# Kernel tuning notes

Hardware: AMD Instinct MI355X
Metric: run time of the kernel (lower is better)

## Reference

```python
import jax, jax.numpy as jnp
import numpy as np

B = 1024
IN_SHAPE = ((8, 8, 8), (8, 8))
IN_RANKS = ((32, 32, 32), (32, 32))
OUT_SHAPE = (16, 16, 16)
OUT_RANK = (32, 32, 32)


def _xavier(key, shape):
    # xavier_normal over axes [0,1] (in) and [2] (out), matching the torch helper
    fan_in = shape[0] * shape[1]
    fan_out = shape[2]
    std = float(np.sqrt(2.0 / (fan_in + fan_out)))
    return jax.random.normal(key, shape, dtype=jnp.float32) * std


def setup_inputs() -> dict:
    key = jax.random.key(0)
    ks = jax.random.split(key, 12)
    x_dims = tuple(d for g in IN_SHAPE for d in g)
    inp = {"x": jax.random.normal(ks[0], (B,) + x_dims, dtype=jnp.float32)}
    # input TT factors, flattened over groups in order (group, mode)
    fac_shapes = []
    for shapes, ranks in zip(IN_SHAPE, IN_RANKS):
        for i in range(len(shapes)):
            r_prev = 1 if i == 0 else ranks[i - 1]
            fac_shapes.append((r_prev, shapes[i], ranks[i]))
    for idx, fs in enumerate(fac_shapes):
        inp[f"f{idx}"] = _xavier(ks[1 + idx], fs)
    # core: (last rank of each group..., output_rank[-1])
    core_shape = tuple(r[-1] for r in IN_RANKS) + (OUT_RANK[-1],)
    fan_in = int(np.prod(core_shape[:-1]))
    std = float(np.sqrt(2.0 / (fan_in + core_shape[-1])))
    inp["core"] = jax.random.normal(ks[6], core_shape, dtype=jnp.float32) * std
    # output TT factors
    for i in range(len(OUT_SHAPE)):
        r_prev = 1 if i == 0 else OUT_RANK[i - 1]
        inp[f"g{i}"] = _xavier(ks[7 + i], (r_prev, OUT_SHAPE[i], OUT_RANK[i]))
    # bias: uniform(-1/sqrt(fan_in), +) with fan_in = total input features
    total_in = int(np.prod([np.prod(s) for s in IN_SHAPE]))
    bound = 1.0 / float(np.sqrt(total_in))
    inp["bias"] = jax.random.uniform(ks[10], OUT_SHAPE, dtype=jnp.float32,
                                     minval=-bound, maxval=bound)
    return inp


def reference(x, f0, f1, f2, f3, f4, core, g0, g1, g2, bias):
    groups = ((f0, f1, f2), (f3, f4))
    Bsz = x.shape[0]
    # T: [B, remaining_modes_flat, accumulated_group_ranks_flat]
    T = x.reshape(Bsz, -1)[:, :, None]
    for facs in groups:
        first = facs[0][0]                       # squeeze dummy rank-1: [n, r]
        n = first.shape[0]
        T = T.reshape(Bsz, n, -1, T.shape[-1])   # [B, n, M', Racc]
        T = jnp.einsum("bnmq,nr->bmqr", T, first)  # [B, M', Racc, r]
        for f in facs[1:]:
            n = f.shape[1]
            T = T.reshape(Bsz, n, -1, T.shape[-2], T.shape[-1])
            T = jnp.einsum("bnmqp,pnr->bmqr", T, f)
        # fold this group's final rank into the accumulated rank axis
        T = T.reshape(Bsz, T.shape[1], -1)
    # all input modes consumed -> T is [B, 1, r1_last*r2_last]
    z = T.reshape(Bsz, -1) @ core.reshape(-1, core.shape[-1])  # [B, Rout]
    # output TT chain -> W[o0, o1, o2, R_last]
    W = g0[0]
    for g in (g1, g2):
        W = jnp.einsum("...p,poq->...oq", W, g)
    R = W.shape[-1]
    out = z @ W.reshape(-1, R).T                 # [B, prod(OUT_SHAPE)]
    out = out.reshape((Bsz,) + OUT_SHAPE)
    return out + bias
```

## Files before the change

### kernel.cpp

```cpp
#include <hip/hip_runtime.h>

#define WS_M2 0
#define WS_N2 16384
#define WS_WT 18432
#define WS_Z  149504

__global__ __launch_bounds__(256) void precompute_kernel(
    const float* __restrict__ f0, const float* __restrict__ f1,
    const float* __restrict__ f2, const float* __restrict__ f3,
    const float* __restrict__ f4, const float* __restrict__ g0,
    const float* __restrict__ g1, const float* __restrict__ g2,
    float* __restrict__ ws)
{
    __shared__ float sA[8192];
    const int t = threadIdx.x;
    const int blk = blockIdx.x;
    if (blk < 8) {
        for (int i = t; i < 2048; i += 256) {
            int a01 = i >> 5, r2 = i & 31;
            int a0 = a01 >> 3, a1 = a01 & 7;
            float s = 0.f;
            #pragma unroll
            for (int r1 = 0; r1 < 32; ++r1)
                s += f0[a0*32 + r1] * f1[r1*256 + a1*32 + r2];
            sA[i] = s;
        }
        __syncthreads();
        for (int i = t; i < 2048; i += 256) {
            int a012 = blk*64 + (i >> 5), r3 = i & 31;
            int a01 = a012 >> 3, a2 = a012 & 7;
            float s = 0.f;
            #pragma unroll
            for (int r2 = 0; r2 < 32; ++r2)
                s += sA[a01*32 + r2] * f2[r2*256 + a2*32 + r3];
            ws[WS_M2 + a012*32 + r3] = s;
        }
    } else if (blk == 8) {
        for (int i = t; i < 2048; i += 256) {
            int a34 = i >> 5, s2 = i & 31;
            int a3 = a34 >> 3, a4 = a34 & 7;
            float s = 0.f;
            #pragma unroll
            for (int s1 = 0; s1 < 32; ++s1)
                s += f3[a3*32 + s1] * f4[s1*256 + a4*32 + s2];
            ws[WS_N2 + i] = s;
        }
    } else {
        const int j = blk - 9;
        for (int i = t; i < 8192; i += 256) {
            int o01 = i >> 5, q = i & 31;
            int o0 = o01 >> 4, o1 = o01 & 15;
            float s = 0.f;
            #pragma unroll
            for (int p = 0; p < 32; ++p)
                s += g0[o0*32 + p] * g1[p*512 + o1*32 + q];
            sA[i] = s;
        }
        __syncthreads();
        for (int i = t; i < 4096; i += 256) {
            int o = j*128 + (i >> 5);
            int r = i & 31;
            int o01 = o >> 4, o2 = o & 15;
            float s = 0.f;
            #pragma unroll
            for (int q = 0; q < 32; ++q)
                s += sA[o01*32 + q] * g2[q*512 + o2*32 + r];
            ws[WS_WT + r*4096 + o] = s;
        }
    }
}

__global__ __launch_bounds__(256, 4) void main_kernel(
    const float* __restrict__ x, const float* __restrict__ core,
    const float* __restrict__ ws, float* __restrict__ zout)
{
    __shared__ float buf[8320];
    __shared__ float spart[512];
    const int t = threadIdx.x;
    const int b = blockIdx.x;
    const int w    = __builtin_amdgcn_readfirstlane(t >> 6);
    const int lane = t & 63;

    const float* __restrict__ xw = x + (size_t)b * 32768 + w * 8192 + lane;
    const float* __restrict__ m2 = ws + WS_M2 + w * 4096;

    float acc[32];
    #pragma unroll
    for (int r = 0; r < 32; ++r) acc[r] = 0.f;

    for (int k0 = 0; k0 < 128; k0 += 8) {
        float xv[8];
        #pragma unroll
        for (int i = 0; i < 8; ++i) xv[i] = xw[(k0 + i) * 64];
        #pragma unroll
        for (int i = 0; i < 8; ++i) {
            const float* __restrict__ mr = m2 + (k0 + i) * 32;
            #pragma unroll
            for (int r = 0; r < 32; ++r) acc[r] += xv[i] * mr[r];
        }
    }

    #pragma unroll
    for (int r = 0; r < 32; ++r) buf[w*2080 + r*65 + lane] = acc[r];
    __syncthreads();

    {
        const int rr = t >> 3;
        const int mb = (t & 7) * 8;
        float s[8];
        #pragma unroll
        for (int i = 0; i < 8; ++i) {
            s[i] = buf[rr*65 + mb + i] + buf[2080 + rr*65 + mb + i]
                 + buf[4160 + rr*65 + mb + i] + buf[6240 + rr*65 + mb + i];
        }
        #pragma unroll
        for (int i = 0; i < 8; ++i) buf[rr*65 + mb + i] = s[i];
    }
    __syncthreads();

    {
        const float4* n24 = (const float4*)(ws + WS_N2);
        float4* d = (float4*)(buf + 4160);
        d[t] = n24[t];
        d[256 + t] = n24[256 + t];
    }
    __syncthreads();

    {
        const int r3  = t >> 3;
        const int s2b = (t & 7) * 4;
        float a0=0.f, a1=0.f, a2=0.f, a3=0.f;
        #pragma unroll 8
        for (int m = 0; m < 64; ++m) {
            float av = buf[r3*65 + m];
            const float* n = &buf[4160 + m*32 + s2b];
            a0 += av*n[0]; a1 += av*n[1]; a2 += av*n[2]; a3 += av*n[3];
        }
        float* d = &buf[6240 + r3*32 + s2b];
        d[0]=a0; d[1]=a1; d[2]=a2; d[3]=a3;
    }
    __syncthreads();

    {
        const int ro2 = t & 15;
        const int kc  = t >> 4;
        const float2* core2 = (const float2*)core;
        float s0 = 0.f, s1 = 0.f;
        const int k0 = kc * 64;
        for (int k = k0; k < k0 + 64; ++k) {
            float tv = buf[6240 + k];
            float2 cv = core2[k*16 + ro2];
            s0 += tv*cv.x; s1 += tv*cv.y;
        }
        spart[kc*32 + ro2*2 + 0] = s0;
        spart[kc*32 + ro2*2 + 1] = s1;
    }
    __syncthreads();
    if (t < 32) {
        float s = 0.f;
        #pragma unroll
        for (int kc = 0; kc < 16; ++kc) s += spart[kc*32 + t];
        zout[b*32 + t] = s;
    }
}

__global__ __launch_bounds__(256) void out_kernel(
    const float* __restrict__ ws, const float* __restrict__ bias,
    float* __restrict__ out)
{
    __shared__ float sW[8192];
    __shared__ float sZt[2176];
    __shared__ float sB[256];
    const int t  = threadIdx.x;
    const int bt = blockIdx.x;
    const int ot = blockIdx.y;

    {
        const float4* wt4 = (const float4*)(ws + WS_WT);
        float4* d = (float4*)sW;
        #pragma unroll
        for (int i = 0; i < 8; ++i) {
            int idx = i*256 + t;
            int ro = idx >> 6, oc = idx & 63;
            d[idx] = wt4[ro*1024 + ot*64 + oc];
        }
    }
    {
        const float4* z4 = (const float4*)(ws + WS_Z) + bt*512;
        #pragma unroll
        for (int i = 0; i < 2; ++i) {
            int idx = i*256 + t;
            int bl = idx >> 3, r4 = idx & 7;
            float4 v = z4[idx];
            sZt[(r4*4 + 0)*68 + bl] = v.x;
            sZt[(r4*4 + 1)*68 + bl] = v.y;
            sZt[(r4*4 + 2)*68 + bl] = v.z;
            sZt[(r4*4 + 3)*68 + bl] = v.w;
        }
    }
    if (t < 64) {
        const float4* b4 = (const float4*)bias + ot*64;
        ((float4*)sB)[t] = b4[t];
    }
    __syncthreads();

    const int oc = t & 63;
    const int bg = t >> 6;
    const float4* sW4 = (const float4*)sW;
    const float4 bv = ((const float4*)sB)[oc];
    float4* out4 = (float4*)out;

    for (int bi = 0; bi < 16; bi += 4) {
        const int bl = bg*16 + bi;
        float4 a0 = bv, a1 = bv, a2 = bv, a3 = bv;
        #pragma unroll
        for (int ro = 0; ro < 32; ++ro) {
            float4 w = sW4[ro*64 + oc];
            float4 z = *(const float4*)&sZt[ro*68 + bl];
            a0.x += z.x*w.x; a0.y += z.x*w.y; a0.z += z.x*w.z; a0.w += z.x*w.w;
            a1.x += z.y*w.x; a1.y += z.y*w.y; a1.z += z.y*w.z; a1.w += z.y*w.w;
            a2.x += z.z*w.x; a2.y += z.z*w.y; a2.z += z.z*w.z; a2.w += z.z*w.w;
            a3.x += z.w*w.x; a3.y += z.w*w.y; a3.z += z.w*w.z; a3.w += z.w*w.w;
        }
        const size_t obase = (size_t)(bt*64 + bl) * 1024 + ot*64 + oc;
        out4[obase + 0*1024] = a0;
        out4[obase + 1*1024] = a1;
        out4[obase + 2*1024] = a2;
        out4[obase + 3*1024] = a3;
    }
}

extern "C" void kernel_launch(void* const* d_in, const int* in_sizes, int n_in,
                              void* d_out, int out_size, void* d_ws, size_t ws_size,
                              hipStream_t stream)
{
    const float* x    = (const float*)d_in[0];
    const float* f0   = (const float*)d_in[1];
    const float* f1   = (const float*)d_in[2];
    const float* f2   = (const float*)d_in[3];
    const float* f3   = (const float*)d_in[4];
    const float* f4   = (const float*)d_in[5];
    const float* core = (const float*)d_in[6];
    const float* g0   = (const float*)d_in[7];
    const float* g1   = (const float*)d_in[8];
    const float* g2   = (const float*)d_in[9];
    const float* bias = (const float*)d_in[10];
    float* ws  = (float*)d_ws;
    float* out = (float*)d_out;

    precompute_kernel<<<41, 256, 0, stream>>>(f0, f1, f2, f3, f4, g0, g1, g2, ws);
    main_kernel<<<1024, 256, 0, stream>>>(x, core, ws, ws + WS_Z);
    out_kernel<<<dim3(16, 16), 256, 0, stream>>>(ws, bias, out);
}
```

Baseline: 264.3 us.

## Double-buffer x and M2 tiles via async global-to-LDS loads with register-blocked outer products

Rewrites the first contraction of main_kernel to stream x and M2 chunks into LDS with global_load_lds async copies, double-buffered across 16 stages. Each thread now computes an 8x8 register tile of outer products split over K across 8 subgroups, followed by a two-pass LDS reduction. The goal is to overlap global loads with compute and raise arithmetic intensity over the per-lane strided global reads. In exchange it uses more LDS and registers, drops occupancy to 2 blocks per SM, and adds a syncthreads per chunk.

Result: no change. 268.5 us (+1.6%).

```diff
diff --git a/kernel.cpp b/kernel.cpp
--- a/kernel.cpp
+++ b/kernel.cpp
@@ -4,6 +4,14 @@
 #define WS_N2 16384
 #define WS_WT 18432
 #define WS_Z  149504
+
+typedef unsigned int u32;
+typedef __attribute__((address_space(3))) u32* lds_u32p;
+typedef const __attribute__((address_space(1))) u32* glb_u32p;
+
+__device__ __forceinline__ void async_cp16(const float* g, float* l) {
+    __builtin_amdgcn_global_load_lds((glb_u32p)g, (lds_u32p)l, 16, 0, 0);
+}
 
 __global__ __launch_bounds__(256) void precompute_kernel(
     const float* __restrict__ f0, const float* __restrict__ f1,
@@ -70,61 +78,99 @@
     }
 }
 
-__global__ __launch_bounds__(256, 4) void main_kernel(
+__global__ __launch_bounds__(256, 2) void main_kernel(
     const float* __restrict__ x, const float* __restrict__ core,
     const float* __restrict__ ws, float* __restrict__ zout)
 {
-    __shared__ float buf[8320];
-    __shared__ float spart[512];
+    __shared__ float buf[14336];
     const int t = threadIdx.x;
     const int b = blockIdx.x;
-    const int w    = __builtin_amdgcn_readfirstlane(t >> 6);
     const int lane = t & 63;
-
-    const float* __restrict__ xw = x + (size_t)b * 32768 + w * 8192 + lane;
-    const float* __restrict__ m2 = ws + WS_M2 + w * 4096;
-
-    float acc[32];
+    const int w = t >> 6;
+    const int s = t >> 5;
+    const int u = t & 31;
+    const int mb = u & 7;
+    const int rb = u >> 3;
+
+    const float* __restrict__ xb = x + (size_t)b * 32768;
+    const float* __restrict__ m2 = ws + WS_M2;
+
+    float acc[8][8];
     #pragma unroll
-    for (int r = 0; r < 32; ++r) acc[r] = 0.f;
-
-    for (int k0 = 0; k0 < 128; k0 += 8) {
-        float xv[8];
-        #pragma unroll
-        for (int i = 0; i < 8; ++i) xv[i] = xw[(k0 + i) * 64];
+    for (int i = 0; i < 8; ++i)
+        #pragma unroll
+        for (int j = 0; j < 8; ++j) acc[i][j] = 0.f;
+
+    {
+        const float* xs = xb;
+        async_cp16(xs + w*512       + lane*4, buf +        w*512);
+        async_cp16(xs + w*512 + 256 + lane*4, buf +        w*512 + 256);
+        async_cp16(m2 + w*256       + lane*4, buf + 2048 + w*256);
+    }
+    __syncthreads();
+
+    for (int c = 0; c < 16; ++c) {
+        const int bb = c & 1;
+        if (c + 1 < 16) {
+            const int nb = bb ^ 1;
+            const float* xs = xb + (c + 1) * 2048;
+            const float* ms = m2 + (c + 1) * 1024;
+            async_cp16(xs + w*512       + lane*4, buf + nb*3072 +        w*512);
+            async_cp16(xs + w*512 + 256 + lane*4, buf + nb*3072 +        w*512 + 256);
+            async_cp16(ms + w*256       + lane*4, buf + nb*3072 + 2048 + w*256);
+        }
+        const float* X = buf + bb*3072;
+        const float* M = buf + bb*3072 + 2048;
+        #pragma unroll
+        for (int kk = 0; kk < 4; ++kk) {
+            const int k = s*4 + kk;
+            float4 xa = *(const float4*)&X[k*64 + mb*8];
+            float4 xc = *(const float4*)&X[k*64 + mb*8 + 4];
+            float4 wa = *(const float4*)&M[k*32 + rb*8];
+            float4 wb = *(const float4*)&M[k*32 + rb*8 + 4];
+            const float xm[8] = {xa.x,xa.y,xa.z,xa.w, xc.x,xc.y,xc.z,xc.w};
+            const float wv[8] = {wa.x,wa.y,wa.z,wa.w, wb.x,wb.y,wb.z,wb.w};
+            #pragma unroll
+            for (int i = 0; i < 8; ++i)
+                #pragma unroll
+                for (int j = 0; j < 8; ++j)
+                    acc[i][j] += xm[i] * wv[j];
+        }
+        __syncthreads();
+    }
+
+    const float4* n24 = (const float4*)(ws + WS_N2);
+    float4 n0 = n24[t*2];
+    float4 n1 = n24[t*2 + 1];
+
+    #pragma unroll
+    for (int p = 0; p < 2; ++p) {
         #pragma unroll
         for (int i = 0; i < 8; ++i) {
-            const float* __restrict__ mr = m2 + (k0 + i) * 32;
-            #pragma unroll
-            for (int r = 0; r < 32; ++r) acc[r] += xv[i] * mr[r];
-        }
-    }
-
-    #pragma unroll
-    for (int r = 0; r < 32; ++r) buf[w*2080 + r*65 + lane] = acc[r];
-    __syncthreads();
-
-    {
-        const int rr = t >> 3;
-        const int mb = (t & 7) * 8;
-        float s[8];
-        #pragma unroll
-        for (int i = 0; i < 8; ++i) {
-            s[i] = buf[rr*65 + mb + i] + buf[2080 + rr*65 + mb + i]
-                 + buf[4160 + rr*65 + mb + i] + buf[6240 + rr*65 + mb + i];
-        }
-        #pragma unroll
-        for (int i = 0; i < 8; ++i) buf[rr*65 + mb + i] = s[i];
-    }
-    __syncthreads();
-
-    {
-        const float4* n24 = (const float4*)(ws + WS_N2);
-        float4* d = (float4*)(buf + 4160);
-        d[t] = n24[t];
-        d[256 + t] = n24[256 + t];
-    }
-    __syncthreads();
+            float4 v = {acc[i][p*4+0], acc[i][p*4+1], acc[i][p*4+2], acc[i][p*4+3]};
+            *(float4*)&buf[6144 + s*1024 + i*128 + u*4] = v;
+        }
+        if (p == 1) {
+            *(float4*)&buf[2176 + t*8]     = n0;
+            *(float4*)&buf[2176 + t*8 + 4] = n1;
+        }
+        __syncthreads();
+        {
+            const int rbb = t >> 6, jj = (t >> 4) & 3, mq = t & 15;
+            const int mbb = mq >> 1, i0 = (mq & 1) * 4;
+            float sum0=0.f, sum1=0.f, sum2=0.f, sum3=0.f;
+            #pragma unroll
+            for (int q = 0; q < 8; ++q) {
+                const float* P = &buf[6144 + q*1024 + (rbb*8 + mbb)*4 + jj];
+                sum0 += P[(i0+0)*128]; sum1 += P[(i0+1)*128];
+                sum2 += P[(i0+2)*128]; sum3 += P[(i0+3)*128];
+            }
+            const int r = rbb*8 + p*4 + jj;
+            float4 v = {sum0, sum1, sum2, sum3};
+            *(float4*)&buf[r*68 + mq*4] = v;
+        }
+        __syncthreads();
+    }
 
     {
         const int r3  = t >> 3;
@@ -132,11 +178,11 @@
         float a0=0.f, a1=0.f, a2=0.f, a3=0.f;
         #pragma unroll 8
         for (int m = 0; m < 64; ++m) {
-            float av = buf[r3*65 + m];
-            const float* n = &buf[4160 + m*32 + s2b];
+            float av = buf[r3*68 + m];
+            const float* n = &buf[2176 + m*32 + s2b];
             a0 += av*n[0]; a1 += av*n[1]; a2 += av*n[2]; a3 += av*n[3];
         }
-        float* d = &buf[6240 + r3*32 + s2b];
+        float* d = &buf[4224 + r3*32 + s2b];
         d[0]=a0; d[1]=a1; d[2]=a2; d[3]=a3;
     }
     __syncthreads();
@@ -148,19 +194,19 @@
         float s0 = 0.f, s1 = 0.f;
         const int k0 = kc * 64;
         for (int k = k0; k < k0 + 64; ++k) {
-            float tv = buf[6240 + k];
+            float tv = buf[4224 + k];
             float2 cv = core2[k*16 + ro2];
             s0 += tv*cv.x; s1 += tv*cv.y;
         }
-        spart[kc*32 + ro2*2 + 0] = s0;
-        spart[kc*32 + ro2*2 + 1] = s1;
+        buf[5248 + kc*32 + ro2*2 + 0] = s0;
+        buf[5248 + kc*32 + ro2*2 + 1] = s1;
     }
     __syncthreads();
     if (t < 32) {
-        float s = 0.f;
-        #pragma unroll
-        for (int kc = 0; kc < 16; ++kc) s += spart[kc*32 + t];
-        zout[b*32 + t] = s;
+        float s2 = 0.f;
+        #pragma unroll
+        for (int kc = 0; kc < 16; ++kc) s2 += buf[5248 + kc*32 + t];
+        zout[b*32 + t] = s2;
     }
 }
 
```

## Split main kernel into register-tiled phase1 and separate contraction kernel

Applied to the files above, without the earlier changes.

The per-batch first contraction (x against the precomputed M2 factor) moves into its own kernel that runs two blocks per sample. Each thread register-tiles 4 m by 2 r with vectorized float4/float2 loads, where before each thread kept a 32-wide accumulator and the block did a cross-wave shared-memory reduction. The two halves' partial results go to workspace, and a second kernel sums them, then does the N2 and core contractions. This aims to raise occupancy and memory-load parallelism on the streaming pass over x, at the cost of an extra launch and a global round-trip for the partial sums.

After: 378.6 us. 1.43x slower.

```diff
diff --git a/kernel.cpp b/kernel.cpp
--- a/kernel.cpp
+++ b/kernel.cpp
@@ -4,6 +4,7 @@
 #define WS_N2 16384
 #define WS_WT 18432
 #define WS_Z  149504
+#define WS_P  182272
 
 __global__ __launch_bounds__(256) void precompute_kernel(
     const float* __restrict__ f0, const float* __restrict__ f1,
@@ -70,59 +71,68 @@
     }
 }
 
-__global__ __launch_bounds__(256, 4) void main_kernel(
-    const float* __restrict__ x, const float* __restrict__ core,
-    const float* __restrict__ ws, float* __restrict__ zout)
-{
-    __shared__ float buf[8320];
-    __shared__ float spart[512];
+__global__ __launch_bounds__(256, 6) void phase1_kernel(
+    const float* __restrict__ x, const float* __restrict__ ws_in,
+    float* __restrict__ ws_out)
+{
+    __shared__ float sm[2048];
+    const int t  = threadIdx.x;
+    const int b  = blockIdx.x >> 1;
+    const int h  = blockIdx.x & 1;
+    const int m4 = t & 15;
+    const int rs = t >> 4;
+
+    const float4* __restrict__ x4 = (const float4*)(x + (size_t)b * 32768) + h*4096;
+    const float2* __restrict__ m2 = (const float2*)(ws_in + WS_M2) + h*4096;
+
+    float a00=0.f,a01=0.f,a10=0.f,a11=0.f,a20=0.f,a21=0.f,a30=0.f,a31=0.f;
+
+    for (int kk = 0; kk < 256; kk += 8) {
+        float4 xv[8]; float2 wv[8];
+        #pragma unroll
+        for (int i = 0; i < 8; ++i) xv[i] = x4[(kk + i)*16 + m4];
+        #pragma unroll
+        for (int i = 0; i < 8; ++i) wv[i] = m2[(kk + i)*16 + rs];
+        #pragma unroll
+        for (int i = 0; i < 8; ++i) {
+            a00 += xv[i].x * wv[i].x; a01 += xv[i].x * wv[i].y;
+            a10 += xv[i].y * wv[i].x; a11 += xv[i].y * wv[i].y;
+            a20 += xv[i].z * wv[i].x; a21 += xv[i].z * wv[i].y;
+            a30 += xv[i].w * wv[i].x; a31 += xv[i].w * wv[i].y;
+        }
+    }
+
+    sm[(m4*4 + 0)*32 + rs*2 + 0] = a00; sm[(m4*4 + 0)*32 + rs*2 + 1] = a01;
+    sm[(m4*4 + 1)*32 + rs*2 + 0] = a10; sm[(m4*4 + 1)*32 + rs*2 + 1] = a11;
+    sm[(m4*4 + 2)*32 + rs*2 + 0] = a20; sm[(m4*4 + 2)*32 + rs*2 + 1] = a21;
+    sm[(m4*4 + 3)*32 + rs*2 + 0] = a30; sm[(m4*4 + 3)*32 + rs*2 + 1] = a31;
+    __syncthreads();
+    float4* p4 = (float4*)(ws_out + WS_P + (size_t)blockIdx.x * 2048);
+    const float4* s4 = (const float4*)sm;
+    p4[t] = s4[t];
+    p4[256 + t] = s4[256 + t];
+}
+
+__global__ __launch_bounds__(256) void phase34_kernel(
+    const float* __restrict__ core, const float* __restrict__ ws,
+    float* __restrict__ zout)
+{
+    __shared__ float buf[5632];
     const int t = threadIdx.x;
     const int b = blockIdx.x;
-    const int w    = __builtin_amdgcn_readfirstlane(t >> 6);
-    const int lane = t & 63;
-
-    const float* __restrict__ xw = x + (size_t)b * 32768 + w * 8192 + lane;
-    const float* __restrict__ m2 = ws + WS_M2 + w * 4096;
-
-    float acc[32];
-    #pragma unroll
-    for (int r = 0; r < 32; ++r) acc[r] = 0.f;
-
-    for (int k0 = 0; k0 < 128; k0 += 8) {
-        float xv[8];
-        #pragma unroll
-        for (int i = 0; i < 8; ++i) xv[i] = xw[(k0 + i) * 64];
-        #pragma unroll
-        for (int i = 0; i < 8; ++i) {
-            const float* __restrict__ mr = m2 + (k0 + i) * 32;
-            #pragma unroll
-            for (int r = 0; r < 32; ++r) acc[r] += xv[i] * mr[r];
-        }
-    }
-
-    #pragma unroll
-    for (int r = 0; r < 32; ++r) buf[w*2080 + r*65 + lane] = acc[r];
-    __syncthreads();
-
-    {
-        const int rr = t >> 3;
-        const int mb = (t & 7) * 8;
-        float s[8];
-        #pragma unroll
-        for (int i = 0; i < 8; ++i) {
-            s[i] = buf[rr*65 + mb + i] + buf[2080 + rr*65 + mb + i]
-                 + buf[4160 + rr*65 + mb + i] + buf[6240 + rr*65 + mb + i];
-        }
-        #pragma unroll
-        for (int i = 0; i < 8; ++i) buf[rr*65 + mb + i] = s[i];
-    }
-    __syncthreads();
-
-    {
+
+    {
+        const float4* p0 = (const float4*)(ws + WS_P + (size_t)(b*2    ) * 2048);
+        const float4* p1 = (const float4*)(ws + WS_P + (size_t)(b*2 + 1) * 2048);
         const float4* n24 = (const float4*)(ws + WS_N2);
-        float4* d = (float4*)(buf + 4160);
-        d[t] = n24[t];
-        d[256 + t] = n24[256 + t];
+        float4* d = (float4*)buf;
+        #pragma unroll
+        for (int i = 0; i < 2; ++i) {
+            float4 u = p0[i*256 + t], v = p1[i*256 + t];
+            u.x+=v.x; u.y+=v.y; u.z+=v.z; u.w+=v.w;
+            d[i*256 + t] = u;
+            d[512 + i*256 + t] = n24[i*256 + t];
+        }
     }
     __syncthreads();
 
@@ -132,11 +142,11 @@
         float a0=0.f, a1=0.f, a2=0.f, a3=0.f;
         #pragma unroll 8
         for (int m = 0; m < 64; ++m) {
-            float av = buf[r3*65 + m];
-            const float* n = &buf[4160 + m*32 + s2b];
+            float av = buf[m*32 + r3];
+            const float* n = &buf[2048 + m*32 + s2b];
             a0 += av*n[0]; a1 += av*n[1]; a2 += av*n[2]; a3 += av*n[3];
         }
-        float* d = &buf[6240 + r3*32 + s2b];
+        float* d = &buf[4096 + r3*32 + s2b];
         d[0]=a0; d[1]=a1; d[2]=a2; d[3]=a3;
     }
     __syncthreads();
@@ -148,18 +158,18 @@
         float s0 = 0.f, s1 = 0.f;
         const int k0 = kc * 64;
         for (int k = k0; k < k0 + 64; ++k) {
-            float tv = buf[6240 + k];
+            float tv = buf[4096 + k];
             float2 cv = core2[k*16 + ro2];
             s0 += tv*cv.x; s1 += tv*cv.y;
         }
-        spart[kc*32 + ro2*2 + 0] = s0;
-        spart[kc*32 + ro2*2 + 1] = s1;
+        buf[5120 + kc*32 + ro2*2 + 0] = s0;
+        buf[5120 + kc*32 + ro2*2 + 1] = s1;
     }
     __syncthreads();
     if (t < 32) {
         float s = 0.f;
         #pragma unroll
-        for (int kc = 0; kc < 16; ++kc) s += spart[kc*32 + t];
+        for (int kc = 0; kc < 16; ++kc) s += buf[5120 + kc*32 + t];
         zout[b*32 + t] = s;
     }
 }
@@ -249,6 +259,7 @@
     float* out = (float*)d_out;
 
     precompute_kernel<<<41, 256, 0, stream>>>(f0, f1, f2, f3, f4, g0, g1, g2, ws);
-    main_kernel<<<1024, 256, 0, stream>>>(x, core, ws, ws + WS_Z);
+    phase1_kernel<<<2048, 256, 0, stream>>>(x, ws, ws);
+    phase34_kernel<<<1024, 256, 0, stream>>>(core, ws, ws + WS_Z);
     out_kernel<<<dim3(16, 16), 256, 0, stream>>>(ws, bias, out);
 }
```
